# Kernel optimization log

Measured on AMD Instinct MI355X. Metric: run time of the kernel, lower is better.

The kernel has to match this reference:

```python
import jax, jax.numpy as jnp
import numpy as np

N_NODES = 20000
N_EDGES = 640000
NUM_FEATURES = 128
HIDDEN = 64
HEADS = 4
NUM_CLASSES = 16
NEG_SLOPE = 0.2  # PyG GATConv default leaky_relu slope


def gat_conv(x, src, dst, W, att_s, att_d, b, num_nodes, concat):
    """PyG-style GATConv (inference: attention dropout is identity).
    x: [N, F_in]; src/dst: [E] (self-loops already included);
    W: [F_in, H*C]; att_s/att_d: [H, C]; b: [H*C] or [C]."""
    H, C = att_s.shape
    h = (x @ W).reshape(num_nodes, H, C)            # [N,H,C]
    a_s = jnp.sum(h * att_s, axis=-1)               # [N,H]
    a_d = jnp.sum(h * att_d, axis=-1)               # [N,H]
    e = jax.nn.leaky_relu(a_s[src] + a_d[dst], NEG_SLOPE)  # [E,H]
    # softmax over incoming edges of each destination node
    emax = jax.ops.segment_max(e, dst, num_segments=num_nodes)  # [N,H]
    ex = jnp.exp(e - emax[dst])
    denom = jax.ops.segment_sum(ex, dst, num_segments=num_nodes)
    alpha = ex / denom[dst]                         # [E,H]
    msg = h[src] * alpha[..., None]                 # [E,H,C]
    out = jax.ops.segment_sum(msg, dst, num_segments=num_nodes)  # [N,H,C]
    out = out.reshape(num_nodes, H * C) if concat else out.mean(axis=1)
    return out + b


def setup_inputs() -> dict:
    key = jax.random.key(0)
    ks = jax.random.split(key, 12)
    d1_in, d1_out = NUM_FEATURES, HEADS * HIDDEN
    d2_in, d2_out = HEADS * HIDDEN, HEADS * HIDDEN
    return {
        "x": jax.random.normal(ks[0], (N_NODES, NUM_FEATURES), dtype=jnp.float32),
        "edge_index": jax.random.randint(ks[1], (2, N_EDGES), 0, N_NODES, dtype=jnp.int64)
        if jax.config.jax_enable_x64 else
        jax.random.randint(ks[1], (2, N_EDGES), 0, N_NODES, dtype=jnp.int32),
        "W1": jax.random.normal(ks[2], (d1_in, d1_out), dtype=jnp.float32) / np.sqrt(d1_in),
        "att_src1": jax.random.normal(ks[3], (HEADS, HIDDEN), dtype=jnp.float32) / np.sqrt(HIDDEN),
        "att_dst1": jax.random.normal(ks[4], (HEADS, HIDDEN), dtype=jnp.float32) / np.sqrt(HIDDEN),
        "b1": jnp.zeros((HEADS * HIDDEN,), dtype=jnp.float32),
        "W2": jax.random.normal(ks[5], (d2_in, d2_out), dtype=jnp.float32) / np.sqrt(d2_in),
        "att_src2": jax.random.normal(ks[6], (HEADS, HIDDEN), dtype=jnp.float32) / np.sqrt(HIDDEN),
        "att_dst2": jax.random.normal(ks[7], (HEADS, HIDDEN), dtype=jnp.float32) / np.sqrt(HIDDEN),
        "b2": jnp.zeros((HIDDEN,), dtype=jnp.float32),
        "Wout": jax.random.normal(ks[8], (HIDDEN, NUM_CLASSES), dtype=jnp.float32) / np.sqrt(HIDDEN),
        "bout": jnp.zeros((NUM_CLASSES,), dtype=jnp.float32),
    }


def reference(x, edge_index, W1, att_src1, att_dst1, b1, W2, att_src2, att_dst2, b2, Wout, bout):
    N = x.shape[0]
    loops = jnp.arange(N, dtype=edge_index.dtype)
    src = jnp.concatenate([edge_index[0], loops])   # PyG add_self_loops=True
    dst = jnp.concatenate([edge_index[1], loops])
    h = gat_conv(x, src, dst, W1, att_src1, att_dst1, b1, N, concat=True)
    h = jax.nn.elu(h)                               # dropout is identity at eval
    h = gat_conv(h, src, dst, W2, att_src2, att_dst2, b2, N, concat=False)
    return h @ Wout + bout
```

## Files before the change

### kernel.cpp

```cpp
#include <hip/hip_runtime.h>
#include <hip/hip_bf16.h>
#include <hip/hip_fp16.h>


#define HEADS 4
#define CDIM 64
#define HC 256

typedef __attribute__((ext_vector_type(8))) short bf16x8;
typedef __attribute__((ext_vector_type(4))) float f32x4;

__device__ __forceinline__ short f32_to_bf16_rne(float v) {
  unsigned u = __float_as_uint(v);
  unsigned r = (u + 0x7FFFu + ((u >> 16) & 1u)) >> 16;
  return (short)r;
}
__device__ __forceinline__ float bf16_bits_to_f32(short s) {
  return __uint_as_float(((unsigned)(unsigned short)s) << 16);
}

__global__ __launch_bounds__(256) void pack_w_kernel(
    const float* __restrict__ W, short* __restrict__ Wt_hi,
    short* __restrict__ Wt_lo, int K, int total) {
  const int i = blockIdx.x * 256 + threadIdx.x;
  if (i >= total) return;
  const int k = i >> 8, n = i & 255;
  const float v = W[i];
  const short hi = f32_to_bf16_rne(v);
  const short lo = f32_to_bf16_rne(v - bf16_bits_to_f32(hi));
  Wt_hi[(size_t)n * K + k] = hi;
  Wt_lo[(size_t)n * K + k] = lo;
}

__global__ __launch_bounds__(128) void gemm_mfma_split(
    const float* __restrict__ A, const short* __restrict__ Wt_hi,
    const short* __restrict__ Wt_lo, __half* __restrict__ h16,
    const float* __restrict__ att_s, const float* __restrict__ att_d,
    float* __restrict__ a_s, float* __restrict__ a_d, int M, int K) {
  __shared__ alignas(16) short As_hi[64 * 32];
  __shared__ alignas(16) short As_lo[64 * 32];
  const int t = threadIdx.x;
  const int wave = t >> 6;
  const int lane = t & 63;
  const int quad = lane >> 4;
  const int m16 = lane & 15;
  const int row0 = blockIdx.x * 64;
  const int col0 = blockIdx.y * 128 + wave * 64;
  const int head = col0 >> 6;

  f32x4 acc[4][4] = {};

  for (int k0 = 0; k0 < K; k0 += 32) {
    if (k0) __syncthreads();
#pragma unroll
    for (int uu = 0; uu < 2; ++uu) {
      const int u = t + uu * 128;
      const int r = u >> 2, seg = u & 3;
      const int gr = row0 + r;
      float vv[8] = {0.f, 0.f, 0.f, 0.f, 0.f, 0.f, 0.f, 0.f};
      if (gr < M) {
        const float* ap = A + (size_t)gr * K + k0 + seg * 8;
        const float4 v0 = *(const float4*)ap;
        const float4 v1 = *(const float4*)(ap + 4);
        vv[0] = v0.x; vv[1] = v0.y; vv[2] = v0.z; vv[3] = v0.w;
        vv[4] = v1.x; vv[5] = v1.y; vv[6] = v1.z; vv[7] = v1.w;
      }
      bf16x8 h8, l8;
#pragma unroll
      for (int j = 0; j < 8; ++j) {
        const short hi = f32_to_bf16_rne(vv[j]);
        h8[j] = hi;
        l8[j] = f32_to_bf16_rne(vv[j] - bf16_bits_to_f32(hi));
      }
      *(bf16x8*)(As_hi + r * 32 + seg * 8) = h8;
      *(bf16x8*)(As_lo + r * 32 + seg * 8) = l8;
    }
    bf16x8 b_hi[4], b_lo[4];
#pragma unroll
    for (int nt = 0; nt < 4; ++nt) {
      const size_t off = (size_t)(col0 + nt * 16 + m16) * K + k0 + quad * 8;
      b_hi[nt] = *(const bf16x8*)(Wt_hi + off);
      b_lo[nt] = *(const bf16x8*)(Wt_lo + off);
    }
    __syncthreads();
    bf16x8 a_hi[4], a_lo[4];
#pragma unroll
    for (int mt = 0; mt < 4; ++mt) {
      const int off = (mt * 16 + m16) * 32 + quad * 8;
      a_hi[mt] = *(const bf16x8*)(As_hi + off);
      a_lo[mt] = *(const bf16x8*)(As_lo + off);
    }
#pragma unroll
    for (int mt = 0; mt < 4; ++mt)
#pragma unroll
      for (int nt = 0; nt < 4; ++nt) {
        acc[mt][nt] = __builtin_amdgcn_mfma_f32_16x16x32_bf16(
            a_hi[mt], b_hi[nt], acc[mt][nt], 0, 0, 0);
        acc[mt][nt] = __builtin_amdgcn_mfma_f32_16x16x32_bf16(
            a_hi[mt], b_lo[nt], acc[mt][nt], 0, 0, 0);
        acc[mt][nt] = __builtin_amdgcn_mfma_f32_16x16x32_bf16(
            a_lo[mt], b_hi[nt], acc[mt][nt], 0, 0, 0);
      }
  }
  float sa[4], da[4];
#pragma unroll
  for (int nt = 0; nt < 4; ++nt) {
    sa[nt] = att_s[col0 + nt * 16 + m16];
    da[nt] = att_d[col0 + nt * 16 + m16];
  }
#pragma unroll
  for (int mt = 0; mt < 4; ++mt)
#pragma unroll
    for (int r = 0; r < 4; ++r) {
      const int gr = row0 + mt * 16 + quad * 4 + r;
      float ps = acc[mt][0][r] * sa[0] + acc[mt][1][r] * sa[1] +
                 acc[mt][2][r] * sa[2] + acc[mt][3][r] * sa[3];
      float pd = acc[mt][0][r] * da[0] + acc[mt][1][r] * da[1] +
                 acc[mt][2][r] * da[2] + acc[mt][3][r] * da[3];
#pragma unroll
      for (int off = 1; off <= 8; off <<= 1) {
        ps += __shfl_xor(ps, off);
        pd += __shfl_xor(pd, off);
      }
      if (gr < M) {
        if (m16 == 0) {
          a_s[gr * HEADS + head] = ps;
          a_d[gr * HEADS + head] = pd;
        }
#pragma unroll
        for (int nt = 0; nt < 4; ++nt)
          h16[(size_t)gr * HC + col0 + nt * 16 + m16] =
              __float2half(acc[mt][nt][r]);
      }
    }
}

__global__ __launch_bounds__(256) void deg_count_kernel(
    const int* __restrict__ dst, int* __restrict__ deg, int E_raw, int Etot) {
  const int e = blockIdx.x * 256 + threadIdx.x;
  if (e >= Etot) return;
  const int d = (e < E_raw) ? dst[e] : (e - E_raw);
  atomicAdd(&deg[d], 1);
}

__global__ __launch_bounds__(256) void scan_block_kernel(
    const int* __restrict__ deg, int* __restrict__ incl,
    int* __restrict__ bsum, int N) {
  __shared__ int sm[256];
  const int t = threadIdx.x;
  const int i = blockIdx.x * 256 + t;
  int v = (i < N) ? deg[i] : 0;
  sm[t] = v;
  __syncthreads();
#pragma unroll
  for (int off = 1; off < 256; off <<= 1) {
    int x = (t >= off) ? sm[t - off] : 0;
    __syncthreads();
    sm[t] += x;
    __syncthreads();
  }
  if (i < N) incl[i] = sm[t];
  if (t == 255) bsum[blockIdx.x] = sm[255];
}

__global__ __launch_bounds__(256) void scan_top_kernel(
    const int* __restrict__ bsum, int* __restrict__ boff, int nb) {
  __shared__ int sm[256];
  const int t = threadIdx.x;
  int v = (t < nb) ? bsum[t] : 0;
  sm[t] = v;
  __syncthreads();
#pragma unroll
  for (int off = 1; off < 256; off <<= 1) {
    int x = (t >= off) ? sm[t - off] : 0;
    __syncthreads();
    sm[t] += x;
    __syncthreads();
  }
  if (t < nb) boff[t] = sm[t] - v;
}

__global__ __launch_bounds__(256) void scan_final_kernel(
    const int* __restrict__ deg, const int* __restrict__ incl,
    const int* __restrict__ boff, int* __restrict__ row_ptr,
    int* __restrict__ cursor, int N, int Etot) {
  const int i = blockIdx.x * 256 + threadIdx.x;
  if (i == 0) row_ptr[N] = Etot;
  if (i >= N) return;
  const int v = boff[blockIdx.x] + incl[i] - deg[i];
  row_ptr[i] = v;
  cursor[i] = v;
}

__global__ __launch_bounds__(256) void csr_scatter_kernel(
    const int* __restrict__ src, const int* __restrict__ dst,
    int* __restrict__ cursor, int* __restrict__ csr_src, int E_raw, int Etot) {
  const int e = blockIdx.x * 256 + threadIdx.x;
  if (e >= Etot) return;
  const int s = (e < E_raw) ? src[e] : (e - E_raw);
  const int d = (e < E_raw) ? dst[e] : (e - E_raw);
  const int pos = atomicAdd(&cursor[d], 1);
  csr_src[pos] = s;
}

__device__ __forceinline__ void acc_edge_f16(float ex, const uint4& u,
                                             float4& A, float4& B) {
  const __half2* hp = (const __half2*)&u;
  float2 f;
  f = __half22float2(hp[0]); A.x += ex * f.x; A.y += ex * f.y;
  f = __half22float2(hp[1]); A.z += ex * f.x; A.w += ex * f.y;
  f = __half22float2(hp[2]); B.x += ex * f.x; B.y += ex * f.y;
  f = __half22float2(hp[3]); B.z += ex * f.x; B.w += ex * f.y;
}

__global__ __launch_bounds__(256) void gat_aggregate_kernel(
    const int* __restrict__ row_ptr, const int* __restrict__ csr_src,
    const __half* __restrict__ h16, const float* __restrict__ a_s,
    const float* __restrict__ a_d, const float* __restrict__ b,
    float* __restrict__ out, int mode) {
  const int bid = blockIdx.x;
  const int hd = bid & 3;
  const int n = (bid >> 2) * 4 + (threadIdx.x >> 6);
  const int lane = threadIdx.x & 63;
  const int q = lane >> 3;
  const int oc = lane & 7;
  const float ad = a_d[n * HEADS + hd];
  const int beg = row_ptr[n];
  const int end = row_ptr[n + 1];
  const char* hbase = (const char*)h16 + hd * 128 + oc * 16;
  const float* asb = a_s + hd;
  float4 accA = {0.f, 0.f, 0.f, 0.f}, accB = {0.f, 0.f, 0.f, 0.f};
  float den = 0.f;
  int i = beg + q;
  for (; i + 8 < end; i += 16) {
    const int s0 = csr_src[i];
    const int s1 = csr_src[i + 8];
    const float as0 = asb[s0 * 4];
    const float as1 = asb[s1 * 4];
    const uint4 u0 = *(const uint4*)(hbase + ((unsigned)s0 << 9));
    const uint4 u1 = *(const uint4*)(hbase + ((unsigned)s1 << 9));
    float a0 = as0 + ad; a0 = (a0 > 0.f) ? a0 : 0.2f * a0;
    float a1 = as1 + ad; a1 = (a1 > 0.f) ? a1 : 0.2f * a1;
    const float e0 = __expf(a0);
    const float e1 = __expf(a1);
    den += e0 + e1;
    acc_edge_f16(e0, u0, accA, accB);
    acc_edge_f16(e1, u1, accA, accB);
  }
  for (; i < end; i += 8) {
    const int s = csr_src[i];
    float a = asb[s * 4] + ad;
    a = (a > 0.f) ? a : 0.2f * a;
    const float ex = __expf(a);
    den += ex;
    const uint4 u = *(const uint4*)(hbase + ((unsigned)s << 9));
    acc_edge_f16(ex, u, accA, accB);
  }
#pragma unroll
  for (int off = 8; off <= 32; off <<= 1) {
    accA.x += __shfl_xor(accA.x, off);
    accA.y += __shfl_xor(accA.y, off);
    accA.z += __shfl_xor(accA.z, off);
    accA.w += __shfl_xor(accA.w, off);
    accB.x += __shfl_xor(accB.x, off);
    accB.y += __shfl_xor(accB.y, off);
    accB.z += __shfl_xor(accB.z, off);
    accB.w += __shfl_xor(accB.w, off);
    den    += __shfl_xor(den, off);
  }
  if (lane < 8) {
    const float inv = 1.f / den;
    float u[8] = {accA.x * inv, accA.y * inv, accA.z * inv, accA.w * inv,
                  accB.x * inv, accB.y * inv, accB.z * inv, accB.w * inv};
    if (mode == 0) {
      const int cb = hd * CDIM + oc * 8;
#pragma unroll
      for (int k = 0; k < 8; ++k) {
        const float t = u[k] + b[cb + k];
        u[k] = (t > 0.f) ? t : (__expf(t) - 1.f);
      }
    }
    float* op = out + (size_t)n * HC + hd * CDIM + oc * 8;
    *(float4*)op = make_float4(u[0], u[1], u[2], u[3]);
    *(float4*)(op + 4) = make_float4(u[4], u[5], u[6], u[7]);
  }
}

__global__ __launch_bounds__(256) void final_fused_kernel(
    const float* __restrict__ agg, const float* __restrict__ b2,
    const float* __restrict__ Wout, const float* __restrict__ bout,
    float* __restrict__ out, int N) {
  const int n = blockIdx.x * 4 + (threadIdx.x >> 6);
  const int c = threadIdx.x & 63;
  if (n >= N) return;
  const float* ar = agg + (size_t)n * HC;
  const float m = 0.25f * (ar[c] + ar[c + 64] + ar[c + 128] + ar[c + 192]) +
                  b2[c];
  const float4* wr = (const float4*)(Wout + c * 16);
  const float4 w0 = wr[0], w1 = wr[1], w2 = wr[2], w3 = wr[3];
  float p[16] = {m * w0.x, m * w0.y, m * w0.z, m * w0.w,
                 m * w1.x, m * w1.y, m * w1.z, m * w1.w,
                 m * w2.x, m * w2.y, m * w2.z, m * w2.w,
                 m * w3.x, m * w3.y, m * w3.z, m * w3.w};
#pragma unroll
  for (int off = 1; off < 64; off <<= 1)
#pragma unroll
    for (int j = 0; j < 16; ++j) p[j] += __shfl_xor(p[j], off);
  if (c == 0) {
    float* op = out + (size_t)n * 16;
    *(float4*)op = make_float4(p[0] + bout[0], p[1] + bout[1],
                               p[2] + bout[2], p[3] + bout[3]);
    *(float4*)(op + 4) = make_float4(p[4] + bout[4], p[5] + bout[5],
                                     p[6] + bout[6], p[7] + bout[7]);
    *(float4*)(op + 8) = make_float4(p[8] + bout[8], p[9] + bout[9],
                                     p[10] + bout[10], p[11] + bout[11]);
    *(float4*)(op + 12) = make_float4(p[12] + bout[12], p[13] + bout[13],
                                      p[14] + bout[14], p[15] + bout[15]);
  }
}

extern "C" void kernel_launch(void* const* d_in, const int* in_sizes, int n_in,
                              void* d_out, int out_size, void* d_ws, size_t ws_size,
                              hipStream_t stream) {
  const float* x      = (const float*)d_in[0];
  const int*   eidx   = (const int*)d_in[1];
  const float* W1     = (const float*)d_in[2];
  const float* att_s1 = (const float*)d_in[3];
  const float* att_d1 = (const float*)d_in[4];
  const float* b1     = (const float*)d_in[5];
  const float* W2     = (const float*)d_in[6];
  const float* att_s2 = (const float*)d_in[7];
  const float* att_d2 = (const float*)d_in[8];
  const float* b2     = (const float*)d_in[9];
  const float* Wout   = (const float*)d_in[10];
  const float* bout   = (const float*)d_in[11];
  float* out          = (float*)d_out;

  const int N     = in_sizes[0] / 128;
  const int E_raw = in_sizes[1] / 2;
  const int Etot  = E_raw + N;
  const int* src = eidx;
  const int* dst = eidx + E_raw;
  const int NB = (N + 255) / 256;

  float* ws = (float*)d_ws;
  float* buf_agg = ws;
  float* buf_as  = buf_agg + (size_t)N * HC;
  float* buf_ad  = buf_as + (size_t)N * HEADS;
  __half* h16    = (__half*)(buf_ad + (size_t)N * HEADS);
  int* deg     = (int*)(h16 + (size_t)N * HC);
  int* incl    = deg + N;
  int* row_ptr = incl + N;
  int* cursor  = row_ptr + (N + 1);
  int* bsum    = cursor + N;
  int* boff    = bsum + NB;
  int* csr_src = boff + NB;
  uintptr_t wp = ((uintptr_t)(csr_src + Etot) + 15) & ~(uintptr_t)15;
  short* wt1_hi = (short*)wp;
  short* wt1_lo = wt1_hi + 256 * 128;
  short* wt2_hi = wt1_lo + 256 * 128;
  short* wt2_lo = wt2_hi + 256 * 256;

  const dim3 blk(256);
  const int g_edge = (Etot + 255) / 256;
  const dim3 g_gemm((N + 63) / 64, 2);
  const dim3 blk_gemm(128);

  pack_w_kernel<<<(128 * 256 + 255) / 256, blk, 0, stream>>>(W1, wt1_hi, wt1_lo,
                                                             128, 128 * 256);
  pack_w_kernel<<<(256 * 256 + 255) / 256, blk, 0, stream>>>(W2, wt2_hi, wt2_lo,
                                                             256, 256 * 256);
  hipMemsetAsync(deg, 0, (size_t)N * sizeof(int), stream);
  deg_count_kernel<<<g_edge, blk, 0, stream>>>(dst, deg, E_raw, Etot);
  scan_block_kernel<<<NB, blk, 0, stream>>>(deg, incl, bsum, N);
  scan_top_kernel<<<1, blk, 0, stream>>>(bsum, boff, NB);
  scan_final_kernel<<<NB, blk, 0, stream>>>(deg, incl, boff, row_ptr, cursor, N, Etot);
  csr_scatter_kernel<<<g_edge, blk, 0, stream>>>(src, dst, cursor, csr_src, E_raw, Etot);

  gemm_mfma_split<<<g_gemm, blk_gemm, 0, stream>>>(
      x, wt1_hi, wt1_lo, h16, att_s1, att_d1, buf_as, buf_ad, N, 128);
  gat_aggregate_kernel<<<N, blk, 0, stream>>>(row_ptr, csr_src, h16, buf_as,
                                              buf_ad, b1, buf_agg, 0);

  gemm_mfma_split<<<g_gemm, blk_gemm, 0, stream>>>(
      buf_agg, wt2_hi, wt2_lo, h16, att_s2, att_d2, buf_as, buf_ad, N, 256);
  gat_aggregate_kernel<<<N, blk, 0, stream>>>(row_ptr, csr_src, h16, buf_as,
                                              buf_ad, b2, buf_agg, 1);

  final_fused_kernel<<<(N + 3) / 4, blk, 0, stream>>>(buf_agg, b2, Wout, bout,
                                                      out, N);
}
```

Baseline: 310.1 us.

## Merge scan kernels, use fma_mix in aggregation, vectorize final projection

Replaces the three-kernel prefix scan with a single 1024-thread block in which each thread does a serial chunk scan before a shared-memory scan. This removes two launches and the intermediate buffers. The aggregation kernel now uses inline v_fma_mix_f32 to multiply-accumulate fp16 features straight into fp32, skipping separate conversions, and uses fmaxf for leaky ReLU. The final kernel maps 16 lanes per node with float4 loads, which cuts the shuffle reduction from six steps to four. The fixed loc[24] array silently limits N to about 24K nodes, and a single-block scan serializes that stage.

```diff
diff --git a/kernel.cpp b/kernel.cpp
--- a/kernel.cpp
+++ b/kernel.cpp
@@ -17,6 +17,20 @@
 }
 __device__ __forceinline__ float bf16_bits_to_f32(short s) {
   return __uint_as_float(((unsigned)(unsigned short)s) << 16);
+}
+
+__device__ __forceinline__ void fma_mix2(float& alo, float& ahi,
+                                         unsigned reg, float ex) {
+  asm("v_fma_mix_f32 %0, %2, %3, %0 op_sel:[0,0,0] op_sel_hi:[1,0,0]\n\t"
+      "v_fma_mix_f32 %1, %2, %3, %1 op_sel:[1,0,0] op_sel_hi:[1,0,0]"
+      : "+v"(alo), "+v"(ahi)
+      : "v"(reg), "v"(ex));
+}
+__device__ __forceinline__ void fma_mix8(float ex, const uint4& u, float* acc) {
+  fma_mix2(acc[0], acc[1], u.x, ex);
+  fma_mix2(acc[2], acc[3], u.y, ex);
+  fma_mix2(acc[4], acc[5], u.z, ex);
+  fma_mix2(acc[6], acc[7], u.w, ex);
 }
 
 __global__ __launch_bounds__(256) void pack_w_kernel(
@@ -143,53 +157,39 @@
   atomicAdd(&deg[d], 1);
 }
 
-__global__ __launch_bounds__(256) void scan_block_kernel(
-    const int* __restrict__ deg, int* __restrict__ incl,
-    int* __restrict__ bsum, int N) {
-  __shared__ int sm[256];
+__global__ __launch_bounds__(1024) void scan_all_kernel(
+    const int* __restrict__ deg, int* __restrict__ row_ptr,
+    int* __restrict__ cursor, int N, int Etot) {
+  __shared__ int sm[1024];
   const int t = threadIdx.x;
-  const int i = blockIdx.x * 256 + t;
-  int v = (i < N) ? deg[i] : 0;
-  sm[t] = v;
+  const int CH = (N + 1023) >> 10;
+  const int base = t * CH;
+  int loc[24];
+  int sum = 0;
+  for (int j = 0; j < CH; ++j) {
+    const int idx = base + j;
+    const int v = (idx < N) ? deg[idx] : 0;
+    loc[j] = sum;
+    sum += v;
+  }
+  sm[t] = sum;
   __syncthreads();
-#pragma unroll
-  for (int off = 1; off < 256; off <<= 1) {
-    int x = (t >= off) ? sm[t - off] : 0;
+  for (int off = 1; off < 1024; off <<= 1) {
+    const int x = (t >= off) ? sm[t - off] : 0;
     __syncthreads();
     sm[t] += x;
     __syncthreads();
   }
-  if (i < N) incl[i] = sm[t];
-  if (t == 255) bsum[blockIdx.x] = sm[255];
-}
-
-__global__ __launch_bounds__(256) void scan_top_kernel(
-    const int* __restrict__ bsum, int* __restrict__ boff, int nb) {
-  __shared__ int sm[256];
-  const int t = threadIdx.x;
-  int v = (t < nb) ? bsum[t] : 0;
-  sm[t] = v;
-  __syncthreads();
-#pragma unroll
-  for (int off = 1; off < 256; off <<= 1) {
-    int x = (t >= off) ? sm[t - off] : 0;
-    __syncthreads();
-    sm[t] += x;
-    __syncthreads();
-  }
-  if (t < nb) boff[t] = sm[t] - v;
-}
-
-__global__ __launch_bounds__(256) void scan_final_kernel(
-    const int* __restrict__ deg, const int* __restrict__ incl,
-    const int* __restrict__ boff, int* __restrict__ row_ptr,
-    int* __restrict__ cursor, int N, int Etot) {
-  const int i = blockIdx.x * 256 + threadIdx.x;
-  if (i == 0) row_ptr[N] = Etot;
-  if (i >= N) return;
-  const int v = boff[blockIdx.x] + incl[i] - deg[i];
-  row_ptr[i] = v;
-  cursor[i] = v;
+  const int excl = sm[t] - sum;
+  for (int j = 0; j < CH; ++j) {
+    const int idx = base + j;
+    if (idx < N) {
+      const int v = excl + loc[j];
+      row_ptr[idx] = v;
+      cursor[idx] = v;
+    }
+  }
+  if (t == 0) row_ptr[N] = Etot;
 }
 
 __global__ __launch_bounds__(256) void csr_scatter_kernel(
@@ -201,16 +201,6 @@
   const int d = (e < E_raw) ? dst[e] : (e - E_raw);
   const int pos = atomicAdd(&cursor[d], 1);
   csr_src[pos] = s;
-}
-
-__device__ __forceinline__ void acc_edge_f16(float ex, const uint4& u,
-                                             float4& A, float4& B) {
-  const __half2* hp = (const __half2*)&u;
-  float2 f;
-  f = __half22float2(hp[0]); A.x += ex * f.x; A.y += ex * f.y;
-  f = __half22float2(hp[1]); A.z += ex * f.x; A.w += ex * f.y;
-  f = __half22float2(hp[2]); B.x += ex * f.x; B.y += ex * f.y;
-  f = __half22float2(hp[3]); B.z += ex * f.x; B.w += ex * f.y;
 }
 
 __global__ __launch_bounds__(256) void gat_aggregate_kernel(
@@ -229,7 +219,7 @@
   const int end = row_ptr[n + 1];
   const char* hbase = (const char*)h16 + hd * 128 + oc * 16;
   const float* asb = a_s + hd;
-  float4 accA = {0.f, 0.f, 0.f, 0.f}, accB = {0.f, 0.f, 0.f, 0.f};
+  float acc[8] = {0.f, 0.f, 0.f, 0.f, 0.f, 0.f, 0.f, 0.f};
   float den = 0.f;
   int i = beg + q;
   for (; i + 8 < end; i += 16) {
@@ -239,45 +229,40 @@
     const float as1 = asb[s1 * 4];
     const uint4 u0 = *(const uint4*)(hbase + ((unsigned)s0 << 9));
     const uint4 u1 = *(const uint4*)(hbase + ((unsigned)s1 << 9));
-    float a0 = as0 + ad; a0 = (a0 > 0.f) ? a0 : 0.2f * a0;
-    float a1 = as1 + ad; a1 = (a1 > 0.f) ? a1 : 0.2f * a1;
+    float a0 = as0 + ad; a0 = fmaxf(a0, 0.2f * a0);
+    float a1 = as1 + ad; a1 = fmaxf(a1, 0.2f * a1);
     const float e0 = __expf(a0);
     const float e1 = __expf(a1);
     den += e0 + e1;
-    acc_edge_f16(e0, u0, accA, accB);
-    acc_edge_f16(e1, u1, accA, accB);
+    fma_mix8(e0, u0, acc);
+    fma_mix8(e1, u1, acc);
   }
   for (; i < end; i += 8) {
     const int s = csr_src[i];
     float a = asb[s * 4] + ad;
-    a = (a > 0.f) ? a : 0.2f * a;
+    a = fmaxf(a, 0.2f * a);
     const float ex = __expf(a);
     den += ex;
     const uint4 u = *(const uint4*)(hbase + ((unsigned)s << 9));
-    acc_edge_f16(ex, u, accA, accB);
+    fma_mix8(ex, u, acc);
   }
 #pragma unroll
   for (int off = 8; off <= 32; off <<= 1) {
-    accA.x += __shfl_xor(accA.x, off);
-    accA.y += __shfl_xor(accA.y, off);
-    accA.z += __shfl_xor(accA.z, off);
-    accA.w += __shfl_xor(accA.w, off);
-    accB.x += __shfl_xor(accB.x, off);
-    accB.y += __shfl_xor(accB.y, off);
-    accB.z += __shfl_xor(accB.z, off);
-    accB.w += __shfl_xor(accB.w, off);
-    den    += __shfl_xor(den, off);
+#pragma unroll
+    for (int k = 0; k < 8; ++k) acc[k] += __shfl_xor(acc[k], off);
+    den += __shfl_xor(den, off);
   }
   if (lane < 8) {
     const float inv = 1.f / den;
-    float u[8] = {accA.x * inv, accA.y * inv, accA.z * inv, accA.w * inv,
-                  accB.x * inv, accB.y * inv, accB.z * inv, accB.w * inv};
+    float u[8];
+#pragma unroll
+    for (int k = 0; k < 8; ++k) u[k] = acc[k] * inv;
     if (mode == 0) {
-      const int cb = hd * CDIM + oc * 8;
+      const float* bb = b + hd * CDIM + oc * 8;
 #pragma unroll
       for (int k = 0; k < 8; ++k) {
-        const float t = u[k] + b[cb + k];
-        u[k] = (t > 0.f) ? t : (__expf(t) - 1.f);
+        const float t0 = u[k] + bb[k];
+        u[k] = (t0 > 0.f) ? t0 : (__expf(t0) - 1.f);
       }
     }
     float* op = out + (size_t)n * HC + hd * CDIM + oc * 8;
@@ -290,23 +275,39 @@
     const float* __restrict__ agg, const float* __restrict__ b2,
     const float* __restrict__ Wout, const float* __restrict__ bout,
     float* __restrict__ out, int N) {
-  const int n = blockIdx.x * 4 + (threadIdx.x >> 6);
-  const int c = threadIdx.x & 63;
+  const int lane = threadIdx.x & 63;
+  const int c4 = lane & 15;
+  const int n = blockIdx.x * 16 + (threadIdx.x >> 6) * 4 + (lane >> 4);
   if (n >= N) return;
-  const float* ar = agg + (size_t)n * HC;
-  const float m = 0.25f * (ar[c] + ar[c + 64] + ar[c + 128] + ar[c + 192]) +
-                  b2[c];
-  const float4* wr = (const float4*)(Wout + c * 16);
-  const float4 w0 = wr[0], w1 = wr[1], w2 = wr[2], w3 = wr[3];
-  float p[16] = {m * w0.x, m * w0.y, m * w0.z, m * w0.w,
-                 m * w1.x, m * w1.y, m * w1.z, m * w1.w,
-                 m * w2.x, m * w2.y, m * w2.z, m * w2.w,
-                 m * w3.x, m * w3.y, m * w3.z, m * w3.w};
-#pragma unroll
-  for (int off = 1; off < 64; off <<= 1)
+  const float* ar = agg + (size_t)n * HC + c4 * 4;
+  const float4 a0 = *(const float4*)ar;
+  const float4 a1 = *(const float4*)(ar + 64);
+  const float4 a2 = *(const float4*)(ar + 128);
+  const float4 a3 = *(const float4*)(ar + 192);
+  const float4 bb = *(const float4*)(b2 + c4 * 4);
+  const float m[4] = {0.25f * (a0.x + a1.x + a2.x + a3.x) + bb.x,
+                      0.25f * (a0.y + a1.y + a2.y + a3.y) + bb.y,
+                      0.25f * (a0.z + a1.z + a2.z + a3.z) + bb.z,
+                      0.25f * (a0.w + a1.w + a2.w + a3.w) + bb.w};
+  float p[16] = {};
+#pragma unroll
+  for (int k = 0; k < 4; ++k) {
+    const float4* wr = (const float4*)(Wout + (c4 * 4 + k) * 16);
+    const float4 w0 = wr[0], w1 = wr[1], w2 = wr[2], w3 = wr[3];
+    p[0] += m[k] * w0.x;  p[1] += m[k] * w0.y;
+    p[2] += m[k] * w0.z;  p[3] += m[k] * w0.w;
+    p[4] += m[k] * w1.x;  p[5] += m[k] * w1.y;
+    p[6] += m[k] * w1.z;  p[7] += m[k] * w1.w;
+    p[8] += m[k] * w2.x;  p[9] += m[k] * w2.y;
+    p[10] += m[k] * w2.z; p[11] += m[k] * w2.w;
+    p[12] += m[k] * w3.x; p[13] += m[k] * w3.y;
+    p[14] += m[k] * w3.z; p[15] += m[k] * w3.w;
+  }
+#pragma unroll
+  for (int off = 1; off <= 8; off <<= 1)
 #pragma unroll
     for (int j = 0; j < 16; ++j) p[j] += __shfl_xor(p[j], off);
-  if (c == 0) {
+  if (c4 == 0) {
     float* op = out + (size_t)n * 16;
     *(float4*)op = make_float4(p[0] + bout[0], p[1] + bout[1],
                                p[2] + bout[2], p[3] + bout[3]);
@@ -341,7 +342,6 @@
   const int Etot  = E_raw + N;
   const int* src = eidx;
   const int* dst = eidx + E_raw;
-  const int NB = (N + 255) / 256;
 
   float* ws = (float*)d_ws;
   float* buf_agg = ws;
@@ -349,12 +349,9 @@
   float* buf_ad  = buf_as + (size_t)N * HEADS;
   __half* h16    = (__half*)(buf_ad + (size_t)N * HEADS);
   int* deg     = (int*)(h16 + (size_t)N * HC);
-  int* incl    = deg + N;
-  int* row_ptr = incl + N;
+  int* row_ptr = deg + N;
   int* cursor  = row_ptr + (N + 1);
-  int* bsum    = cursor + N;
-  int* boff    = bsum + NB;
-  int* csr_src = boff + NB;
+  int* csr_src = cursor + N;
   uintptr_t wp = ((uintptr_t)(csr_src + Etot) + 15) & ~(uintptr_t)15;
   short* wt1_hi = (short*)wp;
   short* wt1_lo = wt1_hi + 256 * 128;
@@ -372,9 +369,7 @@
                                                              256, 256 * 256);
   hipMemsetAsync(deg, 0, (size_t)N * sizeof(int), stream);
   deg_count_kernel<<<g_edge, blk, 0, stream>>>(dst, deg, E_raw, Etot);
-  scan_block_kernel<<<NB, blk, 0, stream>>>(deg, incl, bsum, N);
-  scan_top_kernel<<<1, blk, 0, stream>>>(bsum, boff, NB);
-  scan_final_kernel<<<NB, blk, 0, stream>>>(deg, incl, boff, row_ptr, cursor, N, Etot);
+  scan_all_kernel<<<1, 1024, 0, stream>>>(deg, row_ptr, cursor, N, Etot);
   csr_scatter_kernel<<<g_edge, blk, 0, stream>>>(src, dst, cursor, csr_src, E_raw, Etot);
 
   gemm_mfma_split<<<g_gemm, blk_gemm, 0, stream>>>(
@@ -387,6 +382,6 @@
   gat_aggregate_kernel<<<N, blk, 0, stream>>>(row_ptr, csr_src, h16, buf_as,
                                               buf_ad, b2, buf_agg, 1);
 
-  final_fused_kernel<<<(N + 3) / 4, blk, 0, stream>>>(buf_agg, b2, Wout, bout,
-                                                      out, N);
-}
+  final_fused_kernel<<<(N + 15) / 16, blk, 0, stream>>>(buf_agg, b2, Wout, bout,
+                                                        out, N);
+}
```

After: 323.1 us. 1.04x slower.
